# Kernel tuning notes

Hardware: AMD Instinct MI355X
Metric: run time of the kernel (lower is better)

The kernel has to match this reference:

```python
import jax, jax.numpy as jnp
import numpy as np

T, B, D = 1024, 512, 128
NQ = 8          # n_qubits == hidden_dim
H = NQ


def setup_inputs() -> dict:
    key = jax.random.key(0)
    ks = jax.random.split(key, 13)
    fan_in = D + H
    s = 1.0 / np.sqrt(fan_in)
    def lin(kw, kb):
        W = jax.random.uniform(kw, (NQ, fan_in), jnp.float32, -s, s)
        b = jax.random.uniform(kb, (NQ,), jnp.float32, -s, s)
        return W, b
    Wf, bf = lin(ks[0], ks[1])
    Wi, bi = lin(ks[2], ks[3])
    Wu, bu = lin(ks[4], ks[5])
    Wo, bo = lin(ks[6], ks[7])
    qwf = jax.random.normal(ks[8], (NQ,), jnp.float32)
    qwi = jax.random.normal(ks[9], (NQ,), jnp.float32)
    qwu = jax.random.normal(ks[10], (NQ,), jnp.float32)
    qwo = jax.random.normal(ks[11], (NQ,), jnp.float32)
    inputs = jax.random.normal(ks[12], (T, B, D), jnp.float32)
    return {"inputs": inputs,
            "Wf": Wf, "bf": bf, "Wi": Wi, "bi": bi,
            "Wu": Wu, "bu": bu, "Wo": Wo, "bo": bo,
            "qwf": qwf, "qwi": qwi, "qwu": qwu, "qwo": qwo}


def _qgate(z, qw):
    # Analytic form of the circuit: RX(x_i) then RY(w_i) per wire, CNOT ladder,
    # expval(Z_0). Z_0 commutes with the CNOT ladder, so only wire 0 matters:
    # <Z_0> = cos(x_0) * cos(w_0). Gate = sigmoid(<Z_0>), shape [B].
    return jax.nn.sigmoid(jnp.cos(z[:, 0]) * jnp.cos(qw[0]))


def reference(inputs, Wf, bf, Wi, bi, Wu, bu, Wo, bo, qwf, qwi, qwu, qwo):
    batch = inputs.shape[1]
    hx0 = jnp.zeros((batch, H), inputs.dtype)
    cx0 = jnp.zeros((batch, H), inputs.dtype)

    def step(carry, x):
        hx, cx = carry
        comb = jnp.concatenate([x, hx], axis=1)          # [B, D+H]
        f = _qgate(comb @ Wf.T + bf, qwf)                # [B]
        i = _qgate(comb @ Wi.T + bi, qwi)                # [B]
        g = jnp.tanh(comb @ Wu.T + bu)                   # [B, H]
        o = _qgate(comb @ Wo.T + bo, qwo)                # [B]
        cx = f[:, None] * cx + i[:, None] * g
        hx = o[:, None] * jnp.tanh(cx)
        return (hx, cx), hx

    (hx, cx), outputs = jax.lax.scan(step, (hx0, cx0), inputs)
    return outputs, hx, cx
```

## Files before the change

kernel.cpp:

```cpp
#include <hip/hip_runtime.h>
#include <cstddef>

#define TT 1024
#define BB 512
#define FAN 136

__device__ __forceinline__ float v_exp2 (float x){ float d; asm("v_exp_f32 %0, %1"   : "=v"(d) : "v"(x)); return d; }
__device__ __forceinline__ float v_rcp  (float x){ float d; asm("v_rcp_f32 %0, %1"   : "=v"(d) : "v"(x)); return d; }
__device__ __forceinline__ float v_cosr (float x){ float d; asm("v_cos_f32 %0, %1"   : "=v"(d) : "v"(x)); return d; }
__device__ __forceinline__ float v_fract(float x){ float d; asm("v_fract_f32 %0, %1" : "=v"(d) : "v"(x)); return d; }

__device__ __forceinline__ float fast_cos(float x){
    return v_cosr(v_fract(x * 0.15915494309189535f));
}
__device__ __forceinline__ float fast_sigmoid(float x){
    return v_rcp(1.0f + v_exp2(x * -1.4426950408889634f));
}
__device__ __forceinline__ float fast_tanh(float x){
    return 1.0f - 2.0f * v_rcp(v_exp2(x * 2.8853900817779268f) + 1.0f);
}

template<int CTRL>
__device__ __forceinline__ float dppf(float x){
    return __int_as_float(__builtin_amdgcn_mov_dpp(__float_as_int(x), CTRL, 0xF, 0xF, true));
}
template<int PAT>
__device__ __forceinline__ float swzf(float x){
    return __int_as_float(__builtin_amdgcn_ds_swizzle(__float_as_int(x), PAT));
}

__global__ __launch_bounds__(256) void qlstm_zx2(
    const float* __restrict__ x,
    const float* __restrict__ Wf, const float* __restrict__ bf,
    const float* __restrict__ Wi, const float* __restrict__ bi,
    const float* __restrict__ Wu, const float* __restrict__ bu,
    const float* __restrict__ Wo, const float* __restrict__ bo,
    float* __restrict__ Z)
{
    const int tid = threadIdx.x;
    const int bl  = tid >> 4;
    const int ds  = tid & 15;
    const int t   = blockIdx.x >> 1;
    const int b0  = (blockIdx.x & 1) * 256;

    float w[11][8];
    #pragma unroll
    for (int k = 0; k < 8; ++k) {
        const float4 lo = *reinterpret_cast<const float4*>(Wu + k * FAN + ds * 8);
        const float4 hi = *reinterpret_cast<const float4*>(Wu + k * FAN + ds * 8 + 4);
        w[k][0]=lo.x; w[k][1]=lo.y; w[k][2]=lo.z; w[k][3]=lo.w;
        w[k][4]=hi.x; w[k][5]=hi.y; w[k][6]=hi.z; w[k][7]=hi.w;
    }
    {
        const float4 lo = *reinterpret_cast<const float4*>(Wf + ds * 8);
        const float4 hi = *reinterpret_cast<const float4*>(Wf + ds * 8 + 4);
        w[8][0]=lo.x; w[8][1]=lo.y; w[8][2]=lo.z; w[8][3]=lo.w;
        w[8][4]=hi.x; w[8][5]=hi.y; w[8][6]=hi.z; w[8][7]=hi.w;
    }
    {
        const float4 lo = *reinterpret_cast<const float4*>(Wi + ds * 8);
        const float4 hi = *reinterpret_cast<const float4*>(Wi + ds * 8 + 4);
        w[9][0]=lo.x; w[9][1]=lo.y; w[9][2]=lo.z; w[9][3]=lo.w;
        w[9][4]=hi.x; w[9][5]=hi.y; w[9][6]=hi.z; w[9][7]=hi.w;
    }
    {
        const float4 lo = *reinterpret_cast<const float4*>(Wo + ds * 8);
        const float4 hi = *reinterpret_cast<const float4*>(Wo + ds * 8 + 4);
        w[10][0]=lo.x; w[10][1]=lo.y; w[10][2]=lo.z; w[10][3]=lo.w;
        w[10][4]=hi.x; w[10][5]=hi.y; w[10][6]=hi.z; w[10][7]=hi.w;
    }

    float my_bias = 0.f;
    if (ds <  8) my_bias = bu[ds];
    if (ds ==  8) my_bias = bf[0];
    if (ds ==  9) my_bias = bi[0];
    if (ds == 10) my_bias = bo[0];

    const float* xp = x + ((size_t)(t * BB + b0 + bl)) * 128 + ds * 8;

    for (int it = 0; it < 16; ++it) {
        const int b = b0 + it * 16 + bl;
        const float4 xa = *reinterpret_cast<const float4*>(xp);
        const float4 xb = *reinterpret_cast<const float4*>(xp + 4);
        const float xr[8] = {xa.x, xa.y, xa.z, xa.w, xb.x, xb.y, xb.z, xb.w};

        float acc[11];
        #pragma unroll
        for (int k = 0; k < 11; ++k) {
            float s = 0.f;
            #pragma unroll
            for (int e = 0; e < 8; ++e) s = fmaf(xr[e], w[k][e], s);
            acc[k] = s;
        }
        #pragma unroll
        for (int k = 0; k < 11; ++k) {
            float v = acc[k];
            v += dppf<0xB1>(v);
            v += dppf<0x4E>(v);
            v += swzf<0x101F>(v);
            v += swzf<0x201F>(v);
            acc[k] = v;
        }
        float val = acc[0];
        #pragma unroll
        for (int k = 1; k < 11; ++k) val = (ds == k) ? acc[k] : val;
        val += my_bias;
        if (ds < 11)
            Z[(size_t)t * 6144 + (size_t)(b >> 3) * 96 + ds * 8 + (b & 7)] = val;

        xp += 16 * 128;
    }
}

__global__ __launch_bounds__(64) void qlstm_rec2(
    const float* __restrict__ Z,
    const float* __restrict__ Wf, const float* __restrict__ Wi,
    const float* __restrict__ Wu, const float* __restrict__ Wo,
    const float* __restrict__ qwf, const float* __restrict__ qwi,
    const float* __restrict__ qwo,
    float* __restrict__ out)
{
    const int l = threadIdx.x;
    const int g = l >> 3, j = l & 7;
    const int bid = blockIdx.x;

    float wu_[8], wf_[8], wi_[8], wo_[8];
    #pragma unroll
    for (int m = 0; m < 8; ++m) {
        const int k = j ^ m;
        wu_[m] = Wu[j * FAN + 128 + k];
        wf_[m] = Wf[128 + k];
        wi_[m] = Wi[128 + k];
        wo_[m] = Wo[128 + k];
    }
    const float cqf = fast_cos(qwf[0]);
    const float cqi = fast_cos(qwi[0]);
    const float cqo = fast_cos(qwo[0]);

    float a[8];
    #pragma unroll
    for (int m = 0; m < 8; ++m) a[m] = 0.f;
    float c = 0.f, h = 0.f;

    const float* zb = Z + (size_t)bid * 96;
    const int ou = j * 8 + g;
    const int of = 64 + g, oi = 72 + g, oo = 80 + g;

    float zr[8][4];
    #pragma unroll
    for (int p = 0; p < 8; ++p) {
        const float* s = zb + (size_t)p * 6144;
        zr[p][0] = s[ou]; zr[p][1] = s[of]; zr[p][2] = s[oi]; zr[p][3] = s[oo];
    }

    float* op = out + bid * 64 + l;

    for (int t0 = 0; t0 < TT; t0 += 8) {
        #pragma unroll
        for (int p = 0; p < 8; ++p) {
            const float zu = zr[p][0], zf = zr[p][1], zi = zr[p][2], zo = zr[p][3];
            {
                const int tn = t0 + p + 8;
                const float* s = zb + (size_t)(tn < TT ? tn : TT - 1) * 6144;
                zr[p][0] = s[ou]; zr[p][1] = s[of]; zr[p][2] = s[oi]; zr[p][3] = s[oo];
            }

            float du = zu, df = zf, di = zi, dq = zo;
            #pragma unroll
            for (int m = 0; m < 8; ++m) {
                du = fmaf(a[m], wu_[m], du);
                df = fmaf(a[m], wf_[m], df);
                di = fmaf(a[m], wi_[m], di);
                dq = fmaf(a[m], wo_[m], dq);
            }

            const float f  = fast_sigmoid(fast_cos(df) * cqf);
            const float i_ = fast_sigmoid(fast_cos(di) * cqi);
            const float o_ = fast_sigmoid(fast_cos(dq) * cqo);
            const float gg = fast_tanh(du);

            c = fmaf(f, c, i_ * gg);
            h = o_ * fast_tanh(c);

            *op = h; op += 4096;

            a[0] = h;
            a[1] = dppf<0xB1>(h);
            a[2] = dppf<0x4E>(h);
            a[3] = dppf<0x1B>(h);
            const float h7 = dppf<0x141>(h);
            a[7] = h7;
            a[6] = dppf<0xB1>(h7);
            a[5] = dppf<0x4E>(h7);
            a[4] = dppf<0x1B>(h7);
        }
    }

    out[4194304 + bid * 64 + l] = h;
    out[4198400 + bid * 64 + l] = c;
}

extern "C" void kernel_launch(void* const* d_in, const int* in_sizes, int n_in,
                              void* d_out, int out_size, void* d_ws, size_t ws_size,
                              hipStream_t stream) {
    const float* x   = (const float*)d_in[0];
    const float* Wf  = (const float*)d_in[1];
    const float* bf  = (const float*)d_in[2];
    const float* Wi  = (const float*)d_in[3];
    const float* bi  = (const float*)d_in[4];
    const float* Wu  = (const float*)d_in[5];
    const float* bu  = (const float*)d_in[6];
    const float* Wo  = (const float*)d_in[7];
    const float* bo  = (const float*)d_in[8];
    const float* qwf = (const float*)d_in[9];
    const float* qwi = (const float*)d_in[10];
    const float* qwo = (const float*)d_in[12];
    float* out = (float*)d_out;
    float* Z   = (float*)d_ws;

    qlstm_zx2<<<2048, 256, 0, stream>>>(x, Wf, bf, Wi, bi, Wu, bu, Wo, bo, Z);
    qlstm_rec2<<<64, 64, 0, stream>>>(Z, Wf, Wi, Wu, Wo, qwf, qwi, qwo, out);
}
```

Before: 594.3 us.

## Fuse input projection and recurrence into one kernel with per-timestep ready flags

Merges the input-projection kernel and the recurrent kernel into a single launch. The first 16 blocks run the recurrence while the remaining 1024 blocks each compute one timestep's projections and publish a release flag; recurrent blocks spin on acquire loads before prefetching. The recurrence is remapped so 16 lanes per batch element each compute one gate row with a unified sigmoid/tanh formula and swizzles to gather gates. This is meant to overlap the projection pass with the serial recurrence and drop a launch boundary, at the cost of spin-waiting, a bounded-timeout fallback, and reliance on producer blocks being scheduled.

```diff
diff --git a/kernel.cpp b/kernel.cpp
--- a/kernel.cpp
+++ b/kernel.cpp
@@ -4,6 +4,10 @@
 #define TT 1024
 #define BB 512
 #define FAN 136
+#define ZSTRIDE 6144
+#define FLAGOFF 6142
+#define NRECB 16
+#define DEPTH 16
 
 __device__ __forceinline__ float v_exp2 (float x){ float d; asm("v_exp_f32 %0, %1"   : "=v"(d) : "v"(x)); return d; }
 __device__ __forceinline__ float v_rcp  (float x){ float d; asm("v_rcp_f32 %0, %1"   : "=v"(d) : "v"(x)); return d; }
@@ -13,12 +17,6 @@
 __device__ __forceinline__ float fast_cos(float x){
     return v_cosr(v_fract(x * 0.15915494309189535f));
 }
-__device__ __forceinline__ float fast_sigmoid(float x){
-    return v_rcp(1.0f + v_exp2(x * -1.4426950408889634f));
-}
-__device__ __forceinline__ float fast_tanh(float x){
-    return 1.0f - 2.0f * v_rcp(v_exp2(x * 2.8853900817779268f) + 1.0f);
-}
 
 template<int CTRL>
 __device__ __forceinline__ float dppf(float x){
@@ -29,166 +27,184 @@
     return __int_as_float(__builtin_amdgcn_ds_swizzle(__float_as_int(x), PAT));
 }
 
-__global__ __launch_bounds__(256) void qlstm_zx2(
+__global__ __launch_bounds__(1024) void qlstm_init(unsigned* zw){
+    zw[(size_t)threadIdx.x * ZSTRIDE + FLAGOFF] = 0u;
+}
+
+__global__ __launch_bounds__(512) void qlstm_fused(
     const float* __restrict__ x,
     const float* __restrict__ Wf, const float* __restrict__ bf,
     const float* __restrict__ Wi, const float* __restrict__ bi,
     const float* __restrict__ Wu, const float* __restrict__ bu,
     const float* __restrict__ Wo, const float* __restrict__ bo,
-    float* __restrict__ Z)
-{
-    const int tid = threadIdx.x;
-    const int bl  = tid >> 4;
-    const int ds  = tid & 15;
-    const int t   = blockIdx.x >> 1;
-    const int b0  = (blockIdx.x & 1) * 256;
-
-    float w[11][8];
-    #pragma unroll
-    for (int k = 0; k < 8; ++k) {
-        const float4 lo = *reinterpret_cast<const float4*>(Wu + k * FAN + ds * 8);
-        const float4 hi = *reinterpret_cast<const float4*>(Wu + k * FAN + ds * 8 + 4);
-        w[k][0]=lo.x; w[k][1]=lo.y; w[k][2]=lo.z; w[k][3]=lo.w;
-        w[k][4]=hi.x; w[k][5]=hi.y; w[k][6]=hi.z; w[k][7]=hi.w;
-    }
-    {
-        const float4 lo = *reinterpret_cast<const float4*>(Wf + ds * 8);
-        const float4 hi = *reinterpret_cast<const float4*>(Wf + ds * 8 + 4);
-        w[8][0]=lo.x; w[8][1]=lo.y; w[8][2]=lo.z; w[8][3]=lo.w;
-        w[8][4]=hi.x; w[8][5]=hi.y; w[8][6]=hi.z; w[8][7]=hi.w;
-    }
-    {
-        const float4 lo = *reinterpret_cast<const float4*>(Wi + ds * 8);
-        const float4 hi = *reinterpret_cast<const float4*>(Wi + ds * 8 + 4);
-        w[9][0]=lo.x; w[9][1]=lo.y; w[9][2]=lo.z; w[9][3]=lo.w;
-        w[9][4]=hi.x; w[9][5]=hi.y; w[9][6]=hi.z; w[9][7]=hi.w;
-    }
-    {
-        const float4 lo = *reinterpret_cast<const float4*>(Wo + ds * 8);
-        const float4 hi = *reinterpret_cast<const float4*>(Wo + ds * 8 + 4);
-        w[10][0]=lo.x; w[10][1]=lo.y; w[10][2]=lo.z; w[10][3]=lo.w;
-        w[10][4]=hi.x; w[10][5]=hi.y; w[10][6]=hi.z; w[10][7]=hi.w;
-    }
-
-    float my_bias = 0.f;
-    if (ds <  8) my_bias = bu[ds];
-    if (ds ==  8) my_bias = bf[0];
-    if (ds ==  9) my_bias = bi[0];
-    if (ds == 10) my_bias = bo[0];
-
-    const float* xp = x + ((size_t)(t * BB + b0 + bl)) * 128 + ds * 8;
-
-    for (int it = 0; it < 16; ++it) {
-        const int b = b0 + it * 16 + bl;
-        const float4 xa = *reinterpret_cast<const float4*>(xp);
-        const float4 xb = *reinterpret_cast<const float4*>(xp + 4);
-        const float xr[8] = {xa.x, xa.y, xa.z, xa.w, xb.x, xb.y, xb.z, xb.w};
-
-        float acc[11];
-        #pragma unroll
-        for (int k = 0; k < 11; ++k) {
-            float s = 0.f;
-            #pragma unroll
-            for (int e = 0; e < 8; ++e) s = fmaf(xr[e], w[k][e], s);
-            acc[k] = s;
-        }
-        #pragma unroll
-        for (int k = 0; k < 11; ++k) {
-            float v = acc[k];
-            v += dppf<0xB1>(v);
-            v += dppf<0x4E>(v);
-            v += swzf<0x101F>(v);
-            v += swzf<0x201F>(v);
-            acc[k] = v;
-        }
-        float val = acc[0];
-        #pragma unroll
-        for (int k = 1; k < 11; ++k) val = (ds == k) ? acc[k] : val;
-        val += my_bias;
-        if (ds < 11)
-            Z[(size_t)t * 6144 + (size_t)(b >> 3) * 96 + ds * 8 + (b & 7)] = val;
-
-        xp += 16 * 128;
-    }
-}
-
-__global__ __launch_bounds__(64) void qlstm_rec2(
-    const float* __restrict__ Z,
-    const float* __restrict__ Wf, const float* __restrict__ Wi,
-    const float* __restrict__ Wu, const float* __restrict__ Wo,
     const float* __restrict__ qwf, const float* __restrict__ qwi,
     const float* __restrict__ qwo,
+    float* __restrict__ Z,
     float* __restrict__ out)
 {
-    const int l = threadIdx.x;
-    const int g = l >> 3, j = l & 7;
     const int bid = blockIdx.x;
-
-    float wu_[8], wf_[8], wi_[8], wo_[8];
+    const int tid = threadIdx.x;
+    unsigned* zw = (unsigned*)Z;
+
+    if (bid >= NRECB) {
+        const int t  = bid - NRECB;
+        const int bl = tid >> 4;
+        const int ds = tid & 15;
+
+        float w[11][8];
+        #pragma unroll
+        for (int k = 0; k < 8; ++k) {
+            const float4 lo = *reinterpret_cast<const float4*>(Wu + k * FAN + ds * 8);
+            const float4 hi = *reinterpret_cast<const float4*>(Wu + k * FAN + ds * 8 + 4);
+            w[k][0]=lo.x; w[k][1]=lo.y; w[k][2]=lo.z; w[k][3]=lo.w;
+            w[k][4]=hi.x; w[k][5]=hi.y; w[k][6]=hi.z; w[k][7]=hi.w;
+        }
+        {
+            const float4 lo = *reinterpret_cast<const float4*>(Wf + ds * 8);
+            const float4 hi = *reinterpret_cast<const float4*>(Wf + ds * 8 + 4);
+            w[8][0]=lo.x; w[8][1]=lo.y; w[8][2]=lo.z; w[8][3]=lo.w;
+            w[8][4]=hi.x; w[8][5]=hi.y; w[8][6]=hi.z; w[8][7]=hi.w;
+        }
+        {
+            const float4 lo = *reinterpret_cast<const float4*>(Wi + ds * 8);
+            const float4 hi = *reinterpret_cast<const float4*>(Wi + ds * 8 + 4);
+            w[9][0]=lo.x; w[9][1]=lo.y; w[9][2]=lo.z; w[9][3]=lo.w;
+            w[9][4]=hi.x; w[9][5]=hi.y; w[9][6]=hi.z; w[9][7]=hi.w;
+        }
+        {
+            const float4 lo = *reinterpret_cast<const float4*>(Wo + ds * 8);
+            const float4 hi = *reinterpret_cast<const float4*>(Wo + ds * 8 + 4);
+            w[10][0]=lo.x; w[10][1]=lo.y; w[10][2]=lo.z; w[10][3]=lo.w;
+            w[10][4]=hi.x; w[10][5]=hi.y; w[10][6]=hi.z; w[10][7]=hi.w;
+        }
+
+        float my_bias = 0.f;
+        if (ds <  8) my_bias = bu[ds];
+        if (ds ==  8) my_bias = bf[0];
+        if (ds ==  9) my_bias = bi[0];
+        if (ds == 10) my_bias = bo[0];
+
+        const float* xp = x + ((size_t)t * BB + bl) * 128 + ds * 8;
+        float* zt = Z + (size_t)t * ZSTRIDE;
+
+        for (int it = 0; it < 16; ++it) {
+            const int b = it * 32 + bl;
+            const float4 xa = *reinterpret_cast<const float4*>(xp);
+            const float4 xb = *reinterpret_cast<const float4*>(xp + 4);
+            const float xr[8] = {xa.x, xa.y, xa.z, xa.w, xb.x, xb.y, xb.z, xb.w};
+
+            float acc[11];
+            #pragma unroll
+            for (int k = 0; k < 11; ++k) {
+                float s = 0.f;
+                #pragma unroll
+                for (int e = 0; e < 8; ++e) s = fmaf(xr[e], w[k][e], s);
+                acc[k] = s;
+            }
+            #pragma unroll
+            for (int k = 0; k < 11; ++k) {
+                float v = acc[k];
+                v += dppf<0xB1>(v);
+                v += dppf<0x4E>(v);
+                v += swzf<0x101F>(v);
+                v += swzf<0x201F>(v);
+                acc[k] = v;
+            }
+            float val = acc[0];
+            #pragma unroll
+            for (int k = 1; k < 11; ++k) val = (ds == k) ? acc[k] : val;
+            val += my_bias;
+            if (ds < 11)
+                zt[(b >> 3) * 96 + ds * 8 + (b & 7)] = val;
+
+            xp += 32 * 128;
+        }
+
+        __syncthreads();
+        if (tid == 0)
+            __hip_atomic_store(zw + (size_t)t * ZSTRIDE + FLAGOFF, 1u,
+                               __ATOMIC_RELEASE, __HIP_MEMORY_SCOPE_AGENT);
+        return;
+    }
+
+    const int cid = tid >> 4;
+    const int r   = tid & 15;
+    const int b   = bid * 32 + cid;
+    const int j   = r & 7;
+    const bool isg = (r < 8);
+    const int rw  = (r < 11) ? r : 11;
+
+    const float* Wrow = (r < 8) ? (Wu + r * FAN)
+                      : (r == 8) ? Wf : (r == 9) ? Wi : Wo;
+    float wt[8];
     #pragma unroll
-    for (int m = 0; m < 8; ++m) {
-        const int k = j ^ m;
-        wu_[m] = Wu[j * FAN + 128 + k];
-        wf_[m] = Wf[128 + k];
-        wi_[m] = Wi[128 + k];
-        wo_[m] = Wo[128 + k];
-    }
-    const float cqf = fast_cos(qwf[0]);
-    const float cqi = fast_cos(qwi[0]);
-    const float cqo = fast_cos(qwo[0]);
+    for (int m = 0; m < 8; ++m)
+        wt[m] = (r < 11) ? Wrow[128 + (j ^ m)] : 0.f;
+
+    const float LOG2E = 1.4426950408889634f;
+    float kq = 2.0f * LOG2E, mm = -2.0f, dd = 1.0f;
+    if (!isg) { mm = 1.0f; dd = 0.0f; }
+    if (r == 8)  kq = -LOG2E * fast_cos(qwf[0]);
+    if (r == 9)  kq = -LOG2E * fast_cos(qwi[0]);
+    if (r == 10) kq = -LOG2E * fast_cos(qwo[0]);
+    if (r >  10) kq = -LOG2E;
+
+    const float* zcol = Z + (size_t)(b >> 3) * 96 + rw * 8 + (b & 7);
+
+    auto waitflag = [&](int tw) {
+        int it = 0;
+        while (__hip_atomic_load(zw + (size_t)tw * ZSTRIDE + FLAGOFF,
+                                 __ATOMIC_ACQUIRE, __HIP_MEMORY_SCOPE_AGENT) != 1u) {
+            __builtin_amdgcn_s_sleep(8);
+            if (++it > (1 << 17)) break;
+        }
+    };
+
+    waitflag(r);
+    float zr[DEPTH];
+    #pragma unroll
+    for (int p = 0; p < DEPTH; ++p) zr[p] = zcol[(size_t)p * ZSTRIDE];
 
     float a[8];
     #pragma unroll
     for (int m = 0; m < 8; ++m) a[m] = 0.f;
-    float c = 0.f, h = 0.f;
-
-    const float* zb = Z + (size_t)bid * 96;
-    const int ou = j * 8 + g;
-    const int of = 64 + g, oi = 72 + g, oo = 80 + g;
-
-    float zr[8][4];
-    #pragma unroll
-    for (int p = 0; p < 8; ++p) {
-        const float* s = zb + (size_t)p * 6144;
-        zr[p][0] = s[ou]; zr[p][1] = s[of]; zr[p][2] = s[oi]; zr[p][3] = s[oo];
-    }
-
-    float* op = out + bid * 64 + l;
-
-    for (int t0 = 0; t0 < TT; t0 += 8) {
+    float c = 0.f, hb = 0.f;
+
+    float* op = out + (size_t)b * 8 + j;
+
+    for (int t0 = 0; t0 < TT; t0 += DEPTH) {
+        if (t0 + DEPTH < TT) waitflag(t0 + DEPTH + r);
         #pragma unroll
-        for (int p = 0; p < 8; ++p) {
-            const float zu = zr[p][0], zf = zr[p][1], zi = zr[p][2], zo = zr[p][3];
-            {
-                const int tn = t0 + p + 8;
-                const float* s = zb + (size_t)(tn < TT ? tn : TT - 1) * 6144;
-                zr[p][0] = s[ou]; zr[p][1] = s[of]; zr[p][2] = s[oi]; zr[p][3] = s[oo];
-            }
-
-            float du = zu, df = zf, di = zi, dq = zo;
-            #pragma unroll
-            for (int m = 0; m < 8; ++m) {
-                du = fmaf(a[m], wu_[m], du);
-                df = fmaf(a[m], wf_[m], df);
-                di = fmaf(a[m], wi_[m], di);
-                dq = fmaf(a[m], wo_[m], dq);
-            }
-
-            const float f  = fast_sigmoid(fast_cos(df) * cqf);
-            const float i_ = fast_sigmoid(fast_cos(di) * cqi);
-            const float o_ = fast_sigmoid(fast_cos(dq) * cqo);
-            const float gg = fast_tanh(du);
-
-            c = fmaf(f, c, i_ * gg);
-            h = o_ * fast_tanh(c);
-
-            *op = h; op += 4096;
-
-            a[0] = h;
-            a[1] = dppf<0xB1>(h);
-            a[2] = dppf<0x4E>(h);
-            a[3] = dppf<0x1B>(h);
-            const float h7 = dppf<0x141>(h);
+        for (int p = 0; p < DEPTH; ++p) {
+            const int t = t0 + p;
+            float d = zr[p];
+            const int tn = t0 + DEPTH + p;
+            if (tn < TT) zr[p] = zcol[(size_t)tn * ZSTRIDE];
+
+            #pragma unroll
+            for (int m = 0; m < 8; ++m) d = fmaf(a[m], wt[m], d);
+
+            const float cz  = fast_cos(d);
+            const float arg = (isg ? d : cz) * kq;
+            const float val = fmaf(v_rcp(1.0f + v_exp2(arg)), mm, dd);
+
+            const float fg = swzf<0x110>(val);
+            const float ig = swzf<0x130>(val);
+            const float og = swzf<0x150>(val);
+
+            c = fmaf(fg, c, ig * val);
+            const float e2 = v_exp2(c * (2.0f * LOG2E));
+            const float tc = fmaf(v_rcp(1.0f + e2), -2.0f, 1.0f);
+            const float h  = og * tc;
+
+            if (r < 8) op[(size_t)t * 4096] = h;
+
+            hb = swzf<0x017>(h);
+            a[0] = hb;
+            a[1] = dppf<0xB1>(hb);
+            a[2] = dppf<0x4E>(hb);
+            a[3] = dppf<0x1B>(hb);
+            const float h7 = dppf<0x141>(hb);
             a[7] = h7;
             a[6] = dppf<0xB1>(h7);
             a[5] = dppf<0x4E>(h7);
@@ -196,8 +212,10 @@
         }
     }
 
-    out[4194304 + bid * 64 + l] = h;
-    out[4198400 + bid * 64 + l] = c;
+    if (r < 8) {
+        out[4194304 + (size_t)b * 8 + j] = hb;
+        out[4198400 + (size_t)b * 8 + j] = c;
+    }
 }
 
 extern "C" void kernel_launch(void* const* d_in, const int* in_sizes, int n_in,
@@ -218,6 +236,7 @@
     float* out = (float*)d_out;
     float* Z   = (float*)d_ws;
 
-    qlstm_zx2<<<2048, 256, 0, stream>>>(x, Wf, bf, Wi, bi, Wu, bu, Wo, bo, Z);
-    qlstm_rec2<<<64, 64, 0, stream>>>(Z, Wf, Wi, Wu, Wo, qwf, qwi, qwo, out);
-}
+    qlstm_init<<<1, 1024, 0, stream>>>((unsigned*)Z);
+    qlstm_fused<<<NRECB + TT, 512, 0, stream>>>(
+        x, Wf, bf, Wi, bi, Wu, bu, Wo, bo, qwf, qwi, qwo, Z, out);
+}
```

After: 705.3 us. 18.7% more time.
